# Optimization experiments

Measured on AMD Instinct MI355X. Metric: run time of the kernel, lower is better.

## Reference

```python
import jax, jax.numpy as jnp
import numpy as np

EMBED = 384
N_HEADS = 6
HEAD_SIZE = EMBED // N_HEADS
B, T = 4, 2048
EPS = 1e-5


def _layernorm(x, g, b):
    mu = jnp.mean(x, axis=-1, keepdims=True)
    var = jnp.mean(jnp.square(x - mu), axis=-1, keepdims=True)
    return (x - mu) * jax.lax.rsqrt(var + EPS) * g + b


def setup_inputs() -> dict:
    key = jax.random.key(0)
    ks = jax.random.split(key, 6)
    s = 0.02
    return {
        "x": jax.random.normal(ks[0], (B, T, EMBED), jnp.float32),
        "Wq": jax.random.normal(ks[1], (N_HEADS, HEAD_SIZE, EMBED), jnp.float32) * s,
        "Wo": jax.random.normal(ks[2], (EMBED, EMBED), jnp.float32) * s,
        "bo": jnp.zeros((EMBED,), jnp.float32),
        "W1": jax.random.normal(ks[3], (EMBED, EMBED), jnp.float32) * s,
        "b1": jnp.zeros((EMBED,), jnp.float32),
        "W2": jax.random.normal(ks[4], (EMBED, EMBED), jnp.float32) * s,
        "b2": jnp.zeros((EMBED,), jnp.float32),
        "g1": jnp.ones((EMBED,), jnp.float32),
        "be1": jnp.zeros((EMBED,), jnp.float32),
        "g2": jnp.ones((EMBED,), jnp.float32),
        "be2": jnp.zeros((EMBED,), jnp.float32),
    }


def reference(x, Wq, Wo, bo, W1, b1, W2, b2, g1, be1, g2, be2):
    # NOTE: original Head uses self.query for q, k AND v (a bug we reproduce):
    # q = k = v = x @ Wq^T per head.
    q = jnp.einsum("bte,hde->bhtd", x, Wq)  # [B,H,T,D]
    scale = HEAD_SIZE ** -0.5
    scores = jnp.einsum("bhtd,bhsd->bhts", q, q) * scale  # [B,H,T,T]
    # torch.tril zeros the upper triangle, then masked_fill(tmp==0, -inf)
    tril = jnp.tril(jnp.ones((T, T), bool))
    scores = jnp.where(tril, scores, 0.0)
    scores = jnp.where(scores == 0.0, -jnp.inf, scores)
    attn = jax.nn.softmax(scores, axis=-1)
    head_out = jnp.einsum("bhts,bhsd->bhtd", attn, q)  # [B,H,T,D]
    cat = head_out.transpose(0, 2, 1, 3).reshape(B, T, EMBED)  # concat heads
    sa = cat @ Wo.T + bo
    x = _layernorm(x + sa, g1, be1)
    ff = jax.nn.relu(x @ W1.T + b1) @ W2.T + b2
    return _layernorm(x + ff, g2, be2)
```

## Files before the change

kernel.cpp:

```cpp
#include <hip/hip_runtime.h>
#include <math.h>

#define BB 4
#define TT 2048
#define EE 384
#define HH 6
#define DD 64
#define MM (BB*TT)

typedef __attribute__((ext_vector_type(8))) short bf16x8;
typedef __attribute__((ext_vector_type(4))) float f32x4;

__device__ __forceinline__ unsigned short f2bf(float f) {
    unsigned int u = __float_as_uint(f);
    u = (u + 0x7FFFu + ((u >> 16) & 1u)) >> 16;
    return (unsigned short)u;
}
__device__ __forceinline__ float bf2f(unsigned short u) {
    return __uint_as_float(((unsigned int)u) << 16);
}
__device__ __forceinline__ unsigned int pk2(float a, float b) {
    return (unsigned int)f2bf(a) | ((unsigned int)f2bf(b) << 16);
}

__global__ __launch_bounds__(256) void k_cvt(const float* __restrict__ x,
                                             const float* __restrict__ wq,
                                             const float* __restrict__ wo,
                                             const float* __restrict__ w1,
                                             const float* __restrict__ w2,
                                             unsigned short* __restrict__ xb,
                                             unsigned short* __restrict__ wqb,
                                             unsigned short* __restrict__ wob,
                                             unsigned short* __restrict__ w1b,
                                             unsigned short* __restrict__ w2b)
{
    int bid = blockIdx.x;
    const float* src; unsigned short* dst; int i;
    if (bid < 3072)       { src = x;  dst = xb;  i = bid * 256; }
    else {
        int r = bid - 3072, wi = r / 144, off = (r % 144) * 256;
        const float* s4[4] = {wq, wo, w1, w2};
        unsigned short* d4[4] = {wqb, wob, w1b, w2b};
        src = s4[wi]; dst = d4[wi]; i = off;
    }
    i += threadIdx.x;
    float4 v = ((const float4*)src)[i];
    uint2 o; o.x = pk2(v.x, v.y); o.y = pk2(v.z, v.w);
    ((uint2*)dst)[i] = o;
}

__global__ __launch_bounds__(256, 4) void k_qgemm(const unsigned short* __restrict__ A,
                                                  const unsigned short* __restrict__ W,
                                                  unsigned short* __restrict__ qbf)
{
    const int tid = threadIdx.x;
    const int w = tid >> 6, lane = tid & 63;
    const int fr = lane & 15, quad = lane >> 4;
    const int m0 = blockIdx.x * 16;
    const int n0 = blockIdx.y * 192 + w * 48;
    const unsigned short* Ap = A + (size_t)(m0 + fr) * EE + quad * 8;
    const unsigned short* Wp = W + (size_t)(n0 + fr) * EE + quad * 8;

    f32x4 acc[3];
    #pragma unroll
    for (int nt = 0; nt < 3; nt++) acc[nt] = (f32x4){0.f, 0.f, 0.f, 0.f};

    #pragma unroll
    for (int k0 = 0; k0 < 12; k0++) {
        bf16x8 a = *(const bf16x8*)(Ap + k0 * 32);
        #pragma unroll
        for (int nt = 0; nt < 3; nt++) {
            bf16x8 b = *(const bf16x8*)(Wp + (size_t)nt * 16 * EE + k0 * 32);
            acc[nt] = __builtin_amdgcn_mfma_f32_16x16x32_bf16(a, b, acc[nt], 0, 0, 0);
        }
    }

    const int mrow = m0 + quad * 4;
    #pragma unroll
    for (int nt = 0; nt < 3; nt++) {
        int n = n0 + nt * 16 + fr;
        int h = n >> 6, d = n & 63;
        #pragma unroll
        for (int r = 0; r < 4; r++) {
            int m = mrow + r;
            int b = m >> 11, t = m & 2047;
            qbf[((size_t)(b * HH + h) * TT + t) * DD + d] = f2bf(acc[nt][r]);
        }
    }
}

__global__ __launch_bounds__(256) void k_prep(const unsigned short* __restrict__ qbf,
                                              unsigned short* __restrict__ qbfT)
{
    __shared__ unsigned short Ls[64][72];
    const int bh = blockIdx.y;
    const int t0 = blockIdx.x * 64;
    const unsigned short* src = qbf + ((size_t)bh * TT + t0) * DD;
    {
        int r = threadIdx.x >> 2, c = (threadIdx.x & 3) * 16;
        const unsigned short* p = src + (size_t)r * DD + c;
        *(uint4*)&Ls[r][c]     = *(const uint4*)(p);
        *(uint4*)&Ls[r][c + 8] = *(const uint4*)(p + 8);
    }
    __syncthreads();
    {
        int d = threadIdx.x >> 2, tc = (threadIdx.x & 3) * 16;
        unsigned short tmp[16];
        #pragma unroll
        for (int i = 0; i < 16; i++) tmp[i] = Ls[tc + i][d];
        unsigned short* dst = qbfT + ((size_t)bh * DD + d) * TT + t0 + tc;
        *(uint4*)(dst)     = *(const uint4*)&tmp[0];
        *(uint4*)(dst + 8) = *(const uint4*)&tmp[8];
    }
}

__global__ __launch_bounds__(256, 4) void k_attn(const unsigned short* __restrict__ qbf,
                                                 const unsigned short* __restrict__ qbfT,
                                                 unsigned short* __restrict__ cat)
{
    __shared__ unsigned short Qs[32][72];
    __shared__ unsigned short Ks[2][64][72];
    __shared__ unsigned short Vs[2][64][72];
    __shared__ unsigned short Ps[32][72];
    __shared__ float lsc[32];
    float (*Oc)[68] = (float(*)[68])&Ks[0][0][0];

    const int id = blockIdx.x;
    const int xcd = id & 7, j = id >> 3;
    const int bh = xcd * 3 + (j % 3);
    const int p = j / 3;
    const int bb = bh / HH, hh = bh % HH;
    const int tid = threadIdx.x;
    const int w = tid >> 6, lane = tid & 63;
    const int qhalf = w & 1, keyhalf = w >> 1;
    const int fr = lane & 15, quad = lane >> 4;
    const int fc = quad * 8;
    const unsigned short* qb  = qbf  + (size_t)bh * TT * DD;
    const unsigned short* qtb = qbfT + (size_t)bh * DD * TT;
    const int lr = tid >> 2, lc = (tid & 3) * 16;
    const int qr = tid >> 3, qc = (tid & 7) * 8;

    #pragma unroll 1
    for (int ph = 0; ph < 2; ph++) {
        const int tile = ph ? (63 - p) : p;
        const int m0 = tile * 32;
        const int nkt = (tile >> 1) + 1;

        uint4 kr0, kr1, vr0, vr1;
        {
            const unsigned short* kp = qb + (size_t)lr * DD + lc;
            kr0 = *(const uint4*)(kp);
            kr1 = *(const uint4*)(kp + 8);
            const unsigned short* vp = qtb + (size_t)lr * TT + lc;
            vr0 = *(const uint4*)(vp);
            vr1 = *(const uint4*)(vp + 8);
        }

        __syncthreads();
        {
            const unsigned short* qp = qb + (size_t)(m0 + qr) * DD + qc;
            *(uint4*)&Qs[qr][qc] = *(const uint4*)(qp);
        }
        *(uint4*)&Ks[0][lr][lc]     = kr0;
        *(uint4*)&Ks[0][lr][lc + 8] = kr1;
        *(uint4*)&Vs[0][lr][lc]     = vr0;
        *(uint4*)&Vs[0][lr][lc + 8] = vr1;
        __syncthreads();
        const bf16x8 qA0 = *(const bf16x8*)&Qs[qhalf * 16 + fr][fc];
        const bf16x8 qA1 = *(const bf16x8*)&Qs[qhalf * 16 + fr][fc + 32];

        f32x4 accO[4];
        #pragma unroll
        for (int dt = 0; dt < 4; dt++) accO[dt] = (f32x4){0.f, 0.f, 0.f, 0.f};
        float ls[4] = {0.f, 0.f, 0.f, 0.f};
        const int rowbase = m0 + qhalf * 16 + quad * 4;
        const int prow = qhalf * 16 + quad * 4;

        for (int kt = 0; kt < nkt; kt++) {
            const int cur = kt & 1;
            const int s0 = kt * 64;
            if (kt < nkt - 1) {
                const unsigned short* kp = qb + (size_t)(s0 + 64 + lr) * DD + lc;
                kr0 = *(const uint4*)(kp);
                kr1 = *(const uint4*)(kp + 8);
                const unsigned short* vp = qtb + (size_t)lr * TT + s0 + 64 + lc;
                vr0 = *(const uint4*)(vp);
                vr1 = *(const uint4*)(vp + 8);
            }

            f32x4 S[2];
            #pragma unroll
            for (int nt = 0; nt < 2; nt++) {
                f32x4 acc = (f32x4){0.f, 0.f, 0.f, 0.f};
                bf16x8 b0 = *(const bf16x8*)&Ks[cur][keyhalf * 32 + nt * 16 + fr][fc];
                acc = __builtin_amdgcn_mfma_f32_16x16x32_bf16(qA0, b0, acc, 0, 0, 0);
                bf16x8 b1 = *(const bf16x8*)&Ks[cur][keyhalf * 32 + nt * 16 + fr][fc + 32];
                acc = __builtin_amdgcn_mfma_f32_16x16x32_bf16(qA1, b1, acc, 0, 0, 0);
                S[nt] = acc;
            }

            #pragma unroll
            for (int nt = 0; nt < 2; nt++) {
                int jg = s0 + keyhalf * 32 + nt * 16 + fr;
                #pragma unroll
                for (int r = 0; r < 4; r++) {
                    float v = S[nt][r] * 0.125f;
                    float pv = (jg <= rowbase + r && v != 0.0f) ? __expf(v) : 0.0f;
                    ls[r] += pv;
                    Ps[prow + r][keyhalf * 32 + nt * 16 + fr] = f2bf(pv);
                }
            }

            bf16x8 pA = *(const bf16x8*)&Ps[qhalf * 16 + fr][keyhalf * 32 + fc];
            #pragma unroll
            for (int dt = 0; dt < 4; dt++) {
                bf16x8 v0 = *(const bf16x8*)&Vs[cur][dt * 16 + fr][keyhalf * 32 + fc];
                accO[dt] = __builtin_amdgcn_mfma_f32_16x16x32_bf16(pA, v0, accO[dt], 0, 0, 0);
            }

            if (kt < nkt - 1) {
                *(uint4*)&Ks[cur ^ 1][lr][lc]     = kr0;
                *(uint4*)&Ks[cur ^ 1][lr][lc + 8] = kr1;
                *(uint4*)&Vs[cur ^ 1][lr][lc]     = vr0;
                *(uint4*)&Vs[cur ^ 1][lr][lc + 8] = vr1;
                __syncthreads();
            }
        }

        __syncthreads();
        #pragma unroll
        for (int r = 0; r < 4; r++) {
            #pragma unroll
            for (int o = 1; o < 16; o <<= 1) ls[r] += __shfl_xor(ls[r], o, 64);
        }
        if (keyhalf == 1) {
            #pragma unroll
            for (int dt = 0; dt < 4; dt++)
                #pragma unroll
                for (int r = 0; r < 4; r++)
                    Oc[prow + r][dt * 16 + fr] = accO[dt][r];
            if (fr == 0) {
                #pragma unroll
                for (int r = 0; r < 4; r++) lsc[prow + r] = ls[r];
            }
        }
        __syncthreads();
        if (keyhalf == 0) {
            float lt[4];
            #pragma unroll
            for (int r = 0; r < 4; r++) lt[r] = ls[r] + lsc[prow + r];
            #pragma unroll
            for (int dt = 0; dt < 4; dt++) {
                #pragma unroll
                for (int r = 0; r < 4; r++) {
                    float o = accO[dt][r] + Oc[prow + r][dt * 16 + fr];
                    int t = rowbase + r;
                    cat[((size_t)bb * TT + t) * EE + hh * DD + dt * 16 + fr] =
                        f2bf(o / lt[r]);
                }
            }
        }
    }
}

__global__ __launch_bounds__(512, 2) void k_ffn(const unsigned short* __restrict__ catb,
                                                const unsigned short* __restrict__ wob,
                                                const float* __restrict__ bo,
                                                const float* __restrict__ x,
                                                const float* __restrict__ g1,
                                                const float* __restrict__ be1,
                                                const unsigned short* __restrict__ w1b,
                                                const float* __restrict__ b1,
                                                const unsigned short* __restrict__ w2b,
                                                const float* __restrict__ b2,
                                                const float* __restrict__ g2,
                                                const float* __restrict__ be2,
                                                float* __restrict__ out)
{
    __shared__ unsigned short X1s[32][392];
    __shared__ unsigned short H1s[32][392];
    __shared__ float ssum[32][8];
    __shared__ float ssq[32][8];
    const int tid = threadIdx.x;
    const int w = tid >> 6, lane = tid & 63;
    const int fr = lane & 15, quad = lane >> 4;
    const int m0 = blockIdx.x * 32;
    const int n0 = w * 48;

    f32x4 acc[2][3];
    bf16x8 bc[3], bn[3];

    {
        const unsigned short* Ap0 = catb + (size_t)(m0 + fr) * EE + quad * 8;
        const unsigned short* Ap1 = Ap0 + 16 * EE;
        const unsigned short* Wp = wob + (size_t)(n0 + fr) * EE + quad * 8;
        #pragma unroll
        for (int mt = 0; mt < 2; mt++)
            #pragma unroll
            for (int nt = 0; nt < 3; nt++) acc[mt][nt] = (f32x4){0.f, 0.f, 0.f, 0.f};
        #pragma unroll
        for (int nt = 0; nt < 3; nt++) bc[nt] = *(const bf16x8*)(Wp + (size_t)nt * 16 * EE);
        #pragma unroll
        for (int k0 = 0; k0 < 12; k0++) {
            if (k0 < 11) {
                #pragma unroll
                for (int nt = 0; nt < 3; nt++)
                    bn[nt] = *(const bf16x8*)(Wp + (size_t)nt * 16 * EE + (k0 + 1) * 32);
            }
            bf16x8 a0 = *(const bf16x8*)(Ap0 + k0 * 32);
            bf16x8 a1 = *(const bf16x8*)(Ap1 + k0 * 32);
            #pragma unroll
            for (int nt = 0; nt < 3; nt++) {
                acc[0][nt] = __builtin_amdgcn_mfma_f32_16x16x32_bf16(a0, bc[nt], acc[0][nt], 0, 0, 0);
                acc[1][nt] = __builtin_amdgcn_mfma_f32_16x16x32_bf16(a1, bc[nt], acc[1][nt], 0, 0, 0);
            }
            #pragma unroll
            for (int nt = 0; nt < 3; nt++) bc[nt] = bn[nt];
        }
    }
    {
        float s1[2][4] = {{0.f,0.f,0.f,0.f},{0.f,0.f,0.f,0.f}};
        float s2[2][4] = {{0.f,0.f,0.f,0.f},{0.f,0.f,0.f,0.f}};
        #pragma unroll
        for (int nt = 0; nt < 3; nt++) {
            int n = n0 + nt * 16 + fr;
            float bv = bo[n];
            #pragma unroll
            for (int mt = 0; mt < 2; mt++)
                #pragma unroll
                for (int r = 0; r < 4; r++) {
                    float v = acc[mt][nt][r] + bv
                            + x[(size_t)(m0 + mt * 16 + quad * 4 + r) * EE + n];
                    acc[mt][nt][r] = v;
                    s1[mt][r] += v;
                    s2[mt][r] += v * v;
                }
        }
        #pragma unroll
        for (int mt = 0; mt < 2; mt++)
            #pragma unroll
            for (int r = 0; r < 4; r++) {
                #pragma unroll
                for (int o = 1; o < 16; o <<= 1) {
                    s1[mt][r] += __shfl_xor(s1[mt][r], o, 64);
                    s2[mt][r] += __shfl_xor(s2[mt][r], o, 64);
                }
            }
        if (fr == 0) {
            #pragma unroll
            for (int mt = 0; mt < 2; mt++)
                #pragma unroll
                for (int r = 0; r < 4; r++) {
                    ssum[mt * 16 + quad * 4 + r][w] = s1[mt][r];
                    ssq [mt * 16 + quad * 4 + r][w] = s2[mt][r];
                }
        }
    }
    __syncthreads();
    {
        #pragma unroll
        for (int mt = 0; mt < 2; mt++) {
            float mu[4], rs[4];
            #pragma unroll
            for (int r = 0; r < 4; r++) {
                int row = mt * 16 + quad * 4 + r;
                float t1 = 0.f, t2 = 0.f;
                #pragma unroll
                for (int q = 0; q < 8; q++) { t1 += ssum[row][q]; t2 += ssq[row][q]; }
                mu[r] = t1 * (1.0f / EE);
                float var = t2 * (1.0f / EE) - mu[r] * mu[r];
                rs[r] = rsqrtf(var + 1e-5f);
            }
            #pragma unroll
            for (int nt = 0; nt < 3; nt++) {
                int n = n0 + nt * 16 + fr;
                float gv = g1[n], bev = be1[n];
                #pragma unroll
                for (int r = 0; r < 4; r++) {
                    float v = (acc[mt][nt][r] - mu[r]) * rs[r] * gv + bev;
                    X1s[mt * 16 + quad * 4 + r][n] = f2bf(v);
                }
            }
        }
    }
    __syncthreads();

    {
        const unsigned short* Wp = w1b + (size_t)(n0 + fr) * EE + quad * 8;
        #pragma unroll
        for (int mt = 0; mt < 2; mt++)
            #pragma unroll
            for (int nt = 0; nt < 3; nt++) acc[mt][nt] = (f32x4){0.f, 0.f, 0.f, 0.f};
        #pragma unroll
        for (int nt = 0; nt < 3; nt++) bc[nt] = *(const bf16x8*)(Wp + (size_t)nt * 16 * EE);
        #pragma unroll
        for (int k0 = 0; k0 < 12; k0++) {
            if (k0 < 11) {
                #pragma unroll
                for (int nt = 0; nt < 3; nt++)
                    bn[nt] = *(const bf16x8*)(Wp + (size_t)nt * 16 * EE + (k0 + 1) * 32);
            }
            bf16x8 a0 = *(const bf16x8*)&X1s[fr][k0 * 32 + quad * 8];
            bf16x8 a1 = *(const bf16x8*)&X1s[16 + fr][k0 * 32 + quad * 8];
            #pragma unroll
            for (int nt = 0; nt < 3; nt++) {
                acc[0][nt] = __builtin_amdgcn_mfma_f32_16x16x32_bf16(a0, bc[nt], acc[0][nt], 0, 0, 0);
                acc[1][nt] = __builtin_amdgcn_mfma_f32_16x16x32_bf16(a1, bc[nt], acc[1][nt], 0, 0, 0);
            }
            #pragma unroll
            for (int nt = 0; nt < 3; nt++) bc[nt] = bn[nt];
        }
        #pragma unroll
        for (int nt = 0; nt < 3; nt++) {
            int n = n0 + nt * 16 + fr;
            float bv = b1[n];
            #pragma unroll
            for (int mt = 0; mt < 2; mt++)
                #pragma unroll
                for (int r = 0; r < 4; r++)
                    H1s[mt * 16 + quad * 4 + r][n] = f2bf(fmaxf(acc[mt][nt][r] + bv, 0.0f));
        }
    }
    __syncthreads();

    {
        const unsigned short* Wp = w2b + (size_t)(n0 + fr) * EE + quad * 8;
        #pragma unroll
        for (int mt = 0; mt < 2; mt++)
            #pragma unroll
            for (int nt = 0; nt < 3; nt++) acc[mt][nt] = (f32x4){0.f, 0.f, 0.f, 0.f};
        #pragma unroll
        for (int nt = 0; nt < 3; nt++) bc[nt] = *(const bf16x8*)(Wp + (size_t)nt * 16 * EE);
        #pragma unroll
        for (int k0 = 0; k0 < 12; k0++) {
            if (k0 < 11) {
                #pragma unroll
                for (int nt = 0; nt < 3; nt++)
                    bn[nt] = *(const bf16x8*)(Wp + (size_t)nt * 16 * EE + (k0 + 1) * 32);
            }
            bf16x8 a0 = *(const bf16x8*)&H1s[fr][k0 * 32 + quad * 8];
            bf16x8 a1 = *(const bf16x8*)&H1s[16 + fr][k0 * 32 + quad * 8];
            #pragma unroll
            for (int nt = 0; nt < 3; nt++) {
                acc[0][nt] = __builtin_amdgcn_mfma_f32_16x16x32_bf16(a0, bc[nt], acc[0][nt], 0, 0, 0);
                acc[1][nt] = __builtin_amdgcn_mfma_f32_16x16x32_bf16(a1, bc[nt], acc[1][nt], 0, 0, 0);
            }
            #pragma unroll
            for (int nt = 0; nt < 3; nt++) bc[nt] = bn[nt];
        }
    }
    {
        float s1[2][4] = {{0.f,0.f,0.f,0.f},{0.f,0.f,0.f,0.f}};
        float s2[2][4] = {{0.f,0.f,0.f,0.f},{0.f,0.f,0.f,0.f}};
        #pragma unroll
        for (int nt = 0; nt < 3; nt++) {
            int n = n0 + nt * 16 + fr;
            float bv = b2[n];
            #pragma unroll
            for (int mt = 0; mt < 2; mt++)
                #pragma unroll
                for (int r = 0; r < 4; r++) {
                    float v = acc[mt][nt][r] + bv + bf2f(X1s[mt * 16 + quad * 4 + r][n]);
                    acc[mt][nt][r] = v;
                    s1[mt][r] += v;
                    s2[mt][r] += v * v;
                }
        }
        #pragma unroll
        for (int mt = 0; mt < 2; mt++)
            #pragma unroll
            for (int r = 0; r < 4; r++) {
                #pragma unroll
                for (int o = 1; o < 16; o <<= 1) {
                    s1[mt][r] += __shfl_xor(s1[mt][r], o, 64);
                    s2[mt][r] += __shfl_xor(s2[mt][r], o, 64);
                }
            }
        if (fr == 0) {
            #pragma unroll
            for (int mt = 0; mt < 2; mt++)
                #pragma unroll
                for (int r = 0; r < 4; r++) {
                    ssum[mt * 16 + quad * 4 + r][w] = s1[mt][r];
                    ssq [mt * 16 + quad * 4 + r][w] = s2[mt][r];
                }
        }
    }
    __syncthreads();
    {
        #pragma unroll
        for (int mt = 0; mt < 2; mt++) {
            float mu[4], rs[4];
            #pragma unroll
            for (int r = 0; r < 4; r++) {
                int row = mt * 16 + quad * 4 + r;
                float u1 = 0.f, u2 = 0.f;
                #pragma unroll
                for (int q = 0; q < 8; q++) { u1 += ssum[row][q]; u2 += ssq[row][q]; }
                mu[r] = u1 * (1.0f / EE);
                float var = u2 * (1.0f / EE) - mu[r] * mu[r];
                rs[r] = rsqrtf(var + 1e-5f);
            }
            #pragma unroll
            for (int nt = 0; nt < 3; nt++) {
                int n = n0 + nt * 16 + fr;
                float gv = g2[n], bev = be2[n];
                #pragma unroll
                for (int r = 0; r < 4; r++)
                    out[(size_t)(m0 + mt * 16 + quad * 4 + r) * EE + n] =
                        (acc[mt][nt][r] - mu[r]) * rs[r] * gv + bev;
            }
        }
    }
}

extern "C" void kernel_launch(void* const* d_in, const int* in_sizes, int n_in,
                              void* d_out, int out_size, void* d_ws, size_t ws_size,
                              hipStream_t stream) {
    (void)in_sizes; (void)n_in; (void)out_size; (void)ws_size;
    const float* x   = (const float*)d_in[0];
    const float* Wq  = (const float*)d_in[1];
    const float* Wo  = (const float*)d_in[2];
    const float* bo  = (const float*)d_in[3];
    const float* W1  = (const float*)d_in[4];
    const float* b1  = (const float*)d_in[5];
    const float* W2  = (const float*)d_in[6];
    const float* b2  = (const float*)d_in[7];
    const float* g1  = (const float*)d_in[8];
    const float* be1 = (const float*)d_in[9];
    const float* g2  = (const float*)d_in[10];
    const float* be2 = (const float*)d_in[11];
    float* out = (float*)d_out;

    float* ws = (float*)d_ws;
    const size_t SZ = (size_t)MM * EE;
    float* S1 = ws + SZ;
    float* S2 = ws + 2 * SZ;
    float* S3 = ws + 3 * SZ;

    unsigned short* qbf  = (unsigned short*)S1;
    unsigned short* qbfT = qbf + (size_t)BB * HH * TT * DD;
    unsigned short* catb = (unsigned short*)S2;
    unsigned short* xbf  = (unsigned short*)S3;
    unsigned short* wqb  = xbf + SZ;
    unsigned short* wob  = wqb + (size_t)EE * EE;
    unsigned short* w1b  = wob + (size_t)EE * EE;
    unsigned short* w2b  = w1b + (size_t)EE * EE;

    k_cvt<<<dim3(3072 + 4 * 144), dim3(256), 0, stream>>>(x, Wq, Wo, W1, W2,
                                                          xbf, wqb, wob, w1b, w2b);
    k_qgemm<<<dim3(MM / 16, 2), dim3(256), 0, stream>>>(xbf, wqb, qbf);
    k_prep<<<dim3(TT / 64, BB * HH), dim3(256), 0, stream>>>(qbf, qbfT);
    k_attn<<<dim3(768), dim3(256), 0, stream>>>(qbf, qbfT, catb);
    k_ffn<<<dim3(MM / 32), dim3(512), 0, stream>>>(catb, wob, bo, x, g1, be1,
                                                   w1b, b1, w2b, b2, g2, be2, out);
}
```

Measured before the change: 191.8 us.

## Fuse Q transpose into Q GEMM epilogue and double M tile

Removes the separate k_prep transpose kernel by having the Q projection GEMM stage its bf16 output tile in shared memory and write the transposed copy directly. The GEMM block now covers 32 rows instead of 16, reusing each weight fragment across two MFMAs, and prefetches the next weight fragments into registers. This saves one kernel launch and one global read of the Q buffer, at the cost of extra LDS usage and a lower occupancy bound.

```diff
diff --git a/kernel.cpp b/kernel.cpp
--- a/kernel.cpp
+++ b/kernel.cpp
@@ -49,68 +49,77 @@
     ((uint2*)dst)[i] = o;
 }
 
-__global__ __launch_bounds__(256, 4) void k_qgemm(const unsigned short* __restrict__ A,
+__global__ __launch_bounds__(256, 2) void k_qgemm(const unsigned short* __restrict__ A,
                                                   const unsigned short* __restrict__ W,
-                                                  unsigned short* __restrict__ qbf)
+                                                  unsigned short* __restrict__ qbf,
+                                                  unsigned short* __restrict__ qbfT)
 {
+    __shared__ unsigned short Ts[32][200];
     const int tid = threadIdx.x;
     const int w = tid >> 6, lane = tid & 63;
     const int fr = lane & 15, quad = lane >> 4;
-    const int m0 = blockIdx.x * 16;
+    const int m0 = blockIdx.x * 32;
     const int n0 = blockIdx.y * 192 + w * 48;
-    const unsigned short* Ap = A + (size_t)(m0 + fr) * EE + quad * 8;
+    const unsigned short* Ap0 = A + (size_t)(m0 + fr) * EE + quad * 8;
+    const unsigned short* Ap1 = Ap0 + 16 * EE;
     const unsigned short* Wp = W + (size_t)(n0 + fr) * EE + quad * 8;
 
-    f32x4 acc[3];
+    f32x4 acc[2][3];
+    bf16x8 bc[3], bn[3];
     #pragma unroll
-    for (int nt = 0; nt < 3; nt++) acc[nt] = (f32x4){0.f, 0.f, 0.f, 0.f};
+    for (int mt = 0; mt < 2; mt++)
+        #pragma unroll
+        for (int nt = 0; nt < 3; nt++) acc[mt][nt] = (f32x4){0.f, 0.f, 0.f, 0.f};
+    #pragma unroll
+    for (int nt = 0; nt < 3; nt++) bc[nt] = *(const bf16x8*)(Wp + (size_t)nt * 16 * EE);
 
     #pragma unroll
     for (int k0 = 0; k0 < 12; k0++) {
-        bf16x8 a = *(const bf16x8*)(Ap + k0 * 32);
+        if (k0 < 11) {
+            #pragma unroll
+            for (int nt = 0; nt < 3; nt++)
+                bn[nt] = *(const bf16x8*)(Wp + (size_t)nt * 16 * EE + (k0 + 1) * 32);
+        }
+        bf16x8 a0 = *(const bf16x8*)(Ap0 + k0 * 32);
+        bf16x8 a1 = *(const bf16x8*)(Ap1 + k0 * 32);
         #pragma unroll
         for (int nt = 0; nt < 3; nt++) {
-            bf16x8 b = *(const bf16x8*)(Wp + (size_t)nt * 16 * EE + k0 * 32);
-            acc[nt] = __builtin_amdgcn_mfma_f32_16x16x32_bf16(a, b, acc[nt], 0, 0, 0);
-        }
-    }
-
-    const int mrow = m0 + quad * 4;
+            acc[0][nt] = __builtin_amdgcn_mfma_f32_16x16x32_bf16(a0, bc[nt], acc[0][nt], 0, 0, 0);
+            acc[1][nt] = __builtin_amdgcn_mfma_f32_16x16x32_bf16(a1, bc[nt], acc[1][nt], 0, 0, 0);
+        }
+        #pragma unroll
+        for (int nt = 0; nt < 3; nt++) bc[nt] = bn[nt];
+    }
+
+    const int bglob = m0 >> 11, t0 = m0 & 2047;
     #pragma unroll
     for (int nt = 0; nt < 3; nt++) {
-        int n = n0 + nt * 16 + fr;
+        int nl = w * 48 + nt * 16 + fr;
+        int n = blockIdx.y * 192 + nl;
         int h = n >> 6, d = n & 63;
         #pragma unroll
-        for (int r = 0; r < 4; r++) {
-            int m = mrow + r;
-            int b = m >> 11, t = m & 2047;
-            qbf[((size_t)(b * HH + h) * TT + t) * DD + d] = f2bf(acc[nt][r]);
-        }
-    }
-}
-
-__global__ __launch_bounds__(256) void k_prep(const unsigned short* __restrict__ qbf,
-                                              unsigned short* __restrict__ qbfT)
-{
-    __shared__ unsigned short Ls[64][72];
-    const int bh = blockIdx.y;
-    const int t0 = blockIdx.x * 64;
-    const unsigned short* src = qbf + ((size_t)bh * TT + t0) * DD;
-    {
-        int r = threadIdx.x >> 2, c = (threadIdx.x & 3) * 16;
-        const unsigned short* p = src + (size_t)r * DD + c;
-        *(uint4*)&Ls[r][c]     = *(const uint4*)(p);
-        *(uint4*)&Ls[r][c + 8] = *(const uint4*)(p + 8);
+        for (int mt = 0; mt < 2; mt++)
+            #pragma unroll
+            for (int r = 0; r < 4; r++) {
+                int ml = mt * 16 + quad * 4 + r;
+                unsigned short bf = f2bf(acc[mt][nt][r]);
+                qbf[((size_t)(bglob * HH + h) * TT + t0 + ml) * DD + d] = bf;
+                Ts[ml][nl] = bf;
+            }
     }
     __syncthreads();
-    {
-        int d = threadIdx.x >> 2, tc = (threadIdx.x & 3) * 16;
-        unsigned short tmp[16];
-        #pragma unroll
-        for (int i = 0; i < 16; i++) tmp[i] = Ls[tc + i][d];
-        unsigned short* dst = qbfT + ((size_t)bh * DD + d) * TT + t0 + tc;
-        *(uint4*)(dst)     = *(const uint4*)&tmp[0];
-        *(uint4*)(dst + 8) = *(const uint4*)&tmp[8];
+    if (tid < 192) {
+        int nl = tid;
+        int n = blockIdx.y * 192 + nl;
+        int h = n >> 6, d = n & 63;
+        unsigned short tmp[32];
+        #pragma unroll
+        for (int i = 0; i < 32; i++) tmp[i] = Ts[i][nl];
+        unsigned short* dst = qbfT + ((size_t)(bglob * HH + h) * DD + d) * TT + t0;
+        *(uint4*)(dst)      = *(const uint4*)&tmp[0];
+        *(uint4*)(dst + 8)  = *(const uint4*)&tmp[8];
+        *(uint4*)(dst + 16) = *(const uint4*)&tmp[16];
+        *(uint4*)(dst + 24) = *(const uint4*)&tmp[24];
     }
 }
 
@@ -549,8 +558,7 @@
 
     k_cvt<<<dim3(3072 + 4 * 144), dim3(256), 0, stream>>>(x, Wq, Wo, W1, W2,
                                                           xbf, wqb, wob, w1b, w2b);
-    k_qgemm<<<dim3(MM / 16, 2), dim3(256), 0, stream>>>(xbf, wqb, qbf);
-    k_prep<<<dim3(TT / 64, BB * HH), dim3(256), 0, stream>>>(qbf, qbfT);
+    k_qgemm<<<dim3(MM / 32, 2), dim3(256), 0, stream>>>(xbf, wqb, qbf, qbfT);
     k_attn<<<dim3(768), dim3(256), 0, stream>>>(qbf, qbfT, catb);
     k_ffn<<<dim3(MM / 32), dim3(512), 0, stream>>>(catb, wob, bo, x, g1, be1,
                                                    w1b, b1, w2b, b2, g2, be2, out);
```

Measured after the change: 182.4 us. -4.9%, faster.
